# Performance work log

Measured on AMD Instinct MI355X. Metric: run time of the kernel, lower is better.

## Reference

```python
import jax, jax.numpy as jnp
import numpy as np

N_NODES = 50000
N_EDGES = 1600000
HIDDEN = 1024
NUM_CLASSES = 64


def setup_inputs() -> dict:
    key = jax.random.key(0)
    k1, k2, k3 = jax.random.split(key, 3)
    x = jax.random.normal(k1, (N_NODES, HIDDEN), dtype=jnp.float32)
    edge_index = jax.random.randint(k2, (2, N_EDGES), 0, N_NODES, dtype=jnp.int64)
    # Glorot-style init for the GCNConv linear weight, zero bias (PyG defaults)
    W = jax.random.normal(k3, (HIDDEN, NUM_CLASSES), dtype=jnp.float32) / np.sqrt(HIDDEN)
    b = jnp.zeros((NUM_CLASSES,), dtype=jnp.float32)
    return {"x": x, "edge_index": edge_index, "W": W, "b": b}


def reference(x, edge_index, W, b):
    # GCNConv: add self-loops, symmetric deg^{-1/2} normalization,
    # linear transform, gather-scale-scatter aggregation, bias, then softmax.
    n = x.shape[0]
    loops = jnp.arange(n, dtype=edge_index.dtype)
    src = jnp.concatenate([edge_index[0], loops])  # [E+N]
    dst = jnp.concatenate([edge_index[1], loops])  # [E+N]

    ones = jnp.ones(dst.shape[0], dtype=x.dtype)
    deg = jax.ops.segment_sum(ones, dst, num_segments=n)  # in-degree incl. self-loop
    deg_inv_sqrt = jnp.where(deg > 0, jax.lax.rsqrt(deg), 0.0)
    norm = deg_inv_sqrt[src] * deg_inv_sqrt[dst]  # [E+N]

    h = x @ W  # [N, C] dense GEMM (transform before propagate)
    msgs = h[src] * norm[:, None]  # gather + scale
    out = jax.ops.segment_sum(msgs, dst, num_segments=n) + b  # scatter-add
    return jax.nn.softmax(out, axis=1)
```

## Files before the change

### kernel.cpp

```cpp
#include <hip/hip_runtime.h>
#include <hip/hip_bf16.h>
#include <math.h>

#define HIDDEN 1024
#define NCLS 64
#define NB 196
#define BCAP 10240
#define CHUNK 4096
#define GCAP 4096

typedef __attribute__((ext_vector_type(8))) short short8;
typedef __attribute__((ext_vector_type(4))) float f32x4;

__device__ __forceinline__ short f2bf(float f) {
    __hip_bfloat16 b = __float2bfloat16(f);
    return __builtin_bit_cast(short, b);
}
__device__ __forceinline__ float bf2f(short s) {
    unsigned u = ((unsigned)(unsigned short)s) << 16;
    return __builtin_bit_cast(float, u);
}

__device__ __forceinline__ void async_copy16(void* lds, const void* g) {
    __builtin_amdgcn_global_load_lds(
        (const __attribute__((address_space(1))) unsigned int*)g,
        (__attribute__((address_space(3))) unsigned int*)lds, 16, 0, 0);
}

__global__ __launch_bounds__(256) void bucket_kernel(const int* __restrict__ ei,
                                                     unsigned* __restrict__ pairs,
                                                     int* __restrict__ bcnt, int E) {
    __shared__ int hist[256];
    __shared__ int offs[256];
    __shared__ int cur[256];
    __shared__ int gbase[256];
    __shared__ unsigned stage[CHUNK];
    __shared__ int nz;
    __shared__ int wsum[4];
    const int tid = threadIdx.x;
    const int base = blockIdx.x * CHUNK;
    const int cnt_c = min(CHUNK, E - base);

    if (tid == 0) nz = 0;
    hist[tid] = 0;
    cur[tid] = 0;
    __syncthreads();

    int found = 0;
    for (int j = tid; j < 1024; j += 256) {
        int e = base + j;
        if (e < E) found |= (ei[2 * e + 1] != 0);
    }
    if (found) atomicOr(&nz, 1);
    __syncthreads();
    const int is64 = (nz == 0);

    unsigned pr[16];
    #pragma unroll
    for (int j = 0; j < 16; ++j) {
        int e = base + j * 256 + tid;
        unsigned p = 0xFFFFFFFFu;
        if (e < E) {
            int s = is64 ? ei[2 * e] : ei[e];
            int d = is64 ? ei[2 * (E + e)] : ei[E + e];
            p = (unsigned)s | ((unsigned)d << 16);
            atomicAdd(&hist[d >> 8], 1);
        }
        pr[j] = p;
    }
    __syncthreads();

    int v = hist[tid];
    int incl = v;
    #pragma unroll
    for (int d = 1; d < 64; d <<= 1) {
        int t = __shfl_up(incl, d);
        if ((tid & 63) >= d) incl += t;
    }
    if ((tid & 63) == 63) wsum[tid >> 6] = incl;
    __syncthreads();
    int pre = 0;
    #pragma unroll
    for (int w = 0; w < 4; ++w)
        if (w < (tid >> 6)) pre += wsum[w];
    offs[tid] = pre + incl - v;
    if (tid < NB && v > 0) gbase[tid] = atomicAdd(&bcnt[tid], v);
    __syncthreads();

    #pragma unroll
    for (int j = 0; j < 16; ++j) {
        unsigned p = pr[j];
        if (p != 0xFFFFFFFFu) {
            int b = (int)(p >> 24);
            int pos = offs[b] + atomicAdd(&cur[b], 1);
            stage[pos] = p;
        }
    }
    __syncthreads();
    for (int i = tid; i < cnt_c; i += 256) {
        unsigned p = stage[i];
        int b = (int)(p >> 24);
        pairs[(size_t)b * BCAP + gbase[b] + (i - offs[b])] = p;
    }
}

__global__ __launch_bounds__(256) void degree_kernel(const unsigned* __restrict__ pairs,
                                                     const int* __restrict__ bcnt,
                                                     float* __restrict__ dis, int n) {
    __shared__ int hist[256];
    const int tid = threadIdx.x;
    const int bucket = blockIdx.x;
    hist[tid] = 0;
    __syncthreads();
    const int cb = bcnt[bucket];
    const unsigned* bp = pairs + (size_t)bucket * BCAP;
    for (int i = tid; i < cb; i += 256) {
        unsigned p = bp[i];
        atomicAdd(&hist[(p >> 16) & 255], 1);
    }
    __syncthreads();
    int node = bucket * 256 + tid;
    if (node < n) dis[node] = rsqrtf((float)hist[tid] + 1.0f);
}

__global__ void wprep_kernel(const float* __restrict__ W,
                             short* __restrict__ wt_hi, short* __restrict__ wt_lo) {
    int idx = blockIdx.x * 256 + threadIdx.x;
    int c = idx >> 10;
    int k = idx & 1023;
    float f = W[(size_t)k * NCLS + c];
    short hb = f2bf(f);
    wt_hi[idx] = hb;
    wt_lo[idx] = f2bf(f - bf2f(hb));
}

__global__ __launch_bounds__(256) void gemm_mfma_kernel(const float* __restrict__ x,
                                                        const short* __restrict__ wt_hi,
                                                        const short* __restrict__ wt_lo,
                                                        float* __restrict__ h, int M) {
    __shared__ char smem[16 * 1040 + 8 * 1040 + 8 * 1040];
    char* As = smem;
    char* Bh = smem + 16 * 1040;
    char* Bl = smem + 24 * 1040;

    const int tid = threadIdx.x;
    const int wave = tid >> 6;
    const int lane = tid & 63;
    const int l15 = lane & 15, l4 = lane >> 4;
    const int row0 = blockIdx.x * 64;

    const float* agp[4];
    #pragma unroll
    for (int i = 0; i < 4; ++i) {
        int rg = row0 + (wave * 4 + i) * 4 + (lane >> 4);
        if (rg > M - 1) rg = M - 1;
        int g = (lane & 15) ^ (((lane >> 4) & 3) << 2);
        agp[i] = x + (size_t)rg * HIDDEN + g * 4;
    }
    const short* bhp[2];
    const short* blp[2];
    #pragma unroll
    for (int i = 0; i < 2; ++i) {
        int c = (wave * 2 + i) * 8 + (lane >> 3);
        int g = (lane & 7) ^ ((lane >> 3) & 7);
        bhp[i] = wt_hi + (size_t)c * HIDDEN + g * 8;
        blp[i] = wt_lo + (size_t)c * HIDDEN + g * 8;
    }

    f32x4 acc[4];
    #pragma unroll
    for (int nf = 0; nf < 4; ++nf) acc[nf] = (f32x4){0.f, 0.f, 0.f, 0.f};

    const int rt = wave * 16 + l15;
    const int r3 = rt & 3;
    char* arow = As + (rt >> 2) * 1040 + r3 * 256;

    for (int k0 = 0; k0 < HIDDEN; k0 += 64) {
        #pragma unroll
        for (int i = 0; i < 4; ++i)
            async_copy16(As + (wave * 4 + i) * 1040, agp[i] + k0);
        #pragma unroll
        for (int i = 0; i < 2; ++i) {
            async_copy16(Bh + (wave * 2 + i) * 1040, bhp[i] + k0);
            async_copy16(Bl + (wave * 2 + i) * 1040, blp[i] + k0);
        }
        __syncthreads();

        #pragma unroll
        for (int kk = 0; kk < 2; ++kk) {
            int js = (kk * 8 + l4 * 2) ^ (r3 << 2);
            f32x4 af0 = *reinterpret_cast<const f32x4*>(arow + js * 16);
            f32x4 af1 = *reinterpret_cast<const f32x4*>(arow + js * 16 + 16);
            short8 ah, al;
            #pragma unroll
            for (int j = 0; j < 4; ++j) {
                short hb = f2bf(af0[j]);
                ah[j] = hb;
                al[j] = f2bf(af0[j] - bf2f(hb));
                short hb2 = f2bf(af1[j]);
                ah[j + 4] = hb2;
                al[j + 4] = f2bf(af1[j] - bf2f(hb2));
            }
            #pragma unroll
            for (int nf = 0; nf < 4; ++nf) {
                int c = l15 + 16 * nf;
                int jb = (kk * 4 + l4) ^ (c & 7);
                size_t boff = (size_t)(c >> 3) * 1040 + (c & 7) * 128 + jb * 16;
                short8 bh = *reinterpret_cast<const short8*>(Bh + boff);
                short8 bl = *reinterpret_cast<const short8*>(Bl + boff);
                acc[nf] = __builtin_amdgcn_mfma_f32_16x16x32_bf16(ah, bh, acc[nf], 0, 0, 0);
                acc[nf] = __builtin_amdgcn_mfma_f32_16x16x32_bf16(al, bh, acc[nf], 0, 0, 0);
                acc[nf] = __builtin_amdgcn_mfma_f32_16x16x32_bf16(ah, bl, acc[nf], 0, 0, 0);
            }
        }
        __syncthreads();
    }

    #pragma unroll
    for (int j = 0; j < 4; ++j) {
        int r = row0 + wave * 16 + l4 * 4 + j;
        if (r < M) {
            #pragma unroll
            for (int nf = 0; nf < 4; ++nf) {
                h[(size_t)r * NCLS + l15 + 16 * nf] = acc[nf][j];
            }
        }
    }
}

__global__ __launch_bounds__(256) void agg_kernel(const unsigned* __restrict__ pairs,
                                                  const int* __restrict__ bcnt,
                                                  const float* __restrict__ h,
                                                  const float* __restrict__ dis,
                                                  const float* __restrict__ bias,
                                                  float* __restrict__ out, int n) {
    __shared__ int hist[64];
    __shared__ int offs[64];
    __shared__ int cur[64];
    __shared__ unsigned short ssrc[GCAP];
    __shared__ float swt[GCAP];
    const int tid = threadIdx.x;
    const int bucket = blockIdx.x >> 2;
    const int split = blockIdx.x & 3;
    const int base_node = bucket * 256 + split * 64;
    if (base_node >= n) return;
    if (tid < 64) { hist[tid] = 0; cur[tid] = 0; }
    __syncthreads();
    const int cb = bcnt[bucket];
    const unsigned* bp = pairs + (size_t)bucket * BCAP;
    for (int i = tid; i < cb; i += 256) {
        unsigned p = bp[i];
        int loc = (int)((p >> 16) & 255u);
        if ((loc >> 6) == split) atomicAdd(&hist[loc & 63], 1);
    }
    __syncthreads();
    if (tid == 0) {
        int r = 0;
        #pragma unroll
        for (int k = 0; k < 64; ++k) { offs[k] = r; r += hist[k]; }
    }
    __syncthreads();
    for (int i = tid; i < cb; i += 256) {
        unsigned p = bp[i];
        int loc = (int)((p >> 16) & 255u);
        if ((loc >> 6) == split) {
            int ln = loc & 63;
            int pos = offs[ln] + atomicAdd(&cur[ln], 1);
            if (pos < GCAP) {
                int s = (int)(p & 0xFFFFu);
                ssrc[pos] = (unsigned short)s;
                swt[pos] = dis[s];
            }
        }
    }
    __syncthreads();

    const int wave = tid >> 6;
    const int lane = tid & 63;
    const int q = lane & 15;
    const int g = lane >> 4;
    const f32x4 bv = *reinterpret_cast<const f32x4*>(bias + q * 4);

    for (int t = 0; t < 16; ++t) {
        int ln = wave * 16 + t;
        int node = base_node + ln;
        if (node >= n) continue;
        int len = hist[ln];
        int e0 = offs[ln];
        float di = rsqrtf((float)len + 1.0f);

        f32x4 hs = *reinterpret_cast<const f32x4*>(h + (size_t)node * NCLS + q * 4);
        float selfw = (g == 0) ? di : 0.f;
        f32x4 a = {hs[0] * selfw, hs[1] * selfw, hs[2] * selfw, hs[3] * selfw};
        f32x4 a2 = {0.f, 0.f, 0.f, 0.f};

        for (int i = 0; i < len; i += 8) {
            int i1 = i + g;
            bool v1 = i1 < len;
            int s1 = v1 ? (int)ssrc[e0 + i1] : 0;
            float w1 = v1 ? swt[e0 + i1] : 0.f;
            f32x4 r1 = *reinterpret_cast<const f32x4*>(h + (size_t)s1 * NCLS + q * 4);
            if (i + 4 < len) {
                int i2 = i + 4 + g;
                bool v2 = i2 < len;
                int s2 = v2 ? (int)ssrc[e0 + i2] : 0;
                float w2 = v2 ? swt[e0 + i2] : 0.f;
                f32x4 r2 = *reinterpret_cast<const f32x4*>(h + (size_t)s2 * NCLS + q * 4);
                a2[0] += w2 * r2[0]; a2[1] += w2 * r2[1];
                a2[2] += w2 * r2[2]; a2[3] += w2 * r2[3];
            }
            a[0] += w1 * r1[0]; a[1] += w1 * r1[1];
            a[2] += w1 * r1[2]; a[3] += w1 * r1[3];
        }
        #pragma unroll
        for (int c = 0; c < 4; ++c) {
            float s = a[c] + a2[c];
            s += __shfl_xor(s, 16);
            s += __shfl_xor(s, 32);
            a[c] = s * di + bv[c];
        }
        float m = fmaxf(fmaxf(a[0], a[1]), fmaxf(a[2], a[3]));
        #pragma unroll
        for (int d = 1; d < 16; d <<= 1) m = fmaxf(m, __shfl_xor(m, d));
        f32x4 ex;
        #pragma unroll
        for (int c = 0; c < 4; ++c) ex[c] = __expf(a[c] - m);
        float sum = (ex[0] + ex[1]) + (ex[2] + ex[3]);
        #pragma unroll
        for (int d = 1; d < 16; d <<= 1) sum += __shfl_xor(sum, d);
        float inv = 1.f / sum;
        if (g == 0) {
            f32x4 o = {ex[0] * inv, ex[1] * inv, ex[2] * inv, ex[3] * inv};
            *reinterpret_cast<f32x4*>(out + (size_t)node * NCLS + q * 4) = o;
        }
    }
}

extern "C" void kernel_launch(void* const* d_in, const int* in_sizes, int n_in,
                              void* d_out, int out_size, void* d_ws, size_t ws_size,
                              hipStream_t stream) {
    const float* x    = (const float*)d_in[0];
    const int*   ei   = (const int*)d_in[1];
    const float* W    = (const float*)d_in[2];
    const float* bias = (const float*)d_in[3];
    float* out = (float*)d_out;

    const int n = in_sizes[0] / HIDDEN;
    const int E = in_sizes[1] / 2;

    char* ws = (char*)d_ws;
    size_t off = 0;
    auto alloc = [&](size_t bytes) -> void* {
        void* p = (void*)(ws + off);
        off = (off + bytes + 255) & ~((size_t)255);
        return p;
    };
    int*      bcnt  = (int*)alloc((size_t)NB * 4);
    unsigned* pairs = (unsigned*)alloc((size_t)NB * BCAP * 4);
    float*    dis   = (float*)alloc((size_t)n * 4);
    float*    h     = (float*)alloc((size_t)n * NCLS * 4);
    short*    wt_hi = (short*)alloc((size_t)NCLS * HIDDEN * 2);
    short*    wt_lo = (short*)alloc((size_t)NCLS * HIDDEN * 2);
    (void)ws_size;

    hipMemsetAsync(bcnt, 0, (size_t)NB * 4, stream);

    bucket_kernel<<<(E + CHUNK - 1) / CHUNK, 256, 0, stream>>>(ei, pairs, bcnt, E);
    degree_kernel<<<NB, 256, 0, stream>>>(pairs, bcnt, dis, n);

    wprep_kernel<<<(NCLS * HIDDEN) / 256, 256, 0, stream>>>(W, wt_hi, wt_lo);
    gemm_mfma_kernel<<<(n + 63) / 64, 256, 0, stream>>>(x, wt_hi, wt_lo, h, n);
    agg_kernel<<<NB * 4, 256, 0, stream>>>(pairs, bcnt, h, dis, bias, out, n);
}
```

Measured before the change: 164.1 us.

## Co-schedule GEMM and edge bucketing in one launch, store h as fp16

Merges the GEMM and edge-bucketing kernels into one launch that branches on block index, so the memory-bound x read and the edge sort can overlap on the GPU. The intermediate h is now stored in fp16, which halves its write traffic and the gather traffic in aggregation. The aggregation loop switches to 8 lanes per row with 8 channels each. The fp16 h adds rounding error to the result, and the shared-memory buffer is now sized for the larger of the two bodies.

```diff
diff --git a/kernel.cpp b/kernel.cpp
--- a/kernel.cpp
+++ b/kernel.cpp
@@ -1,5 +1,6 @@
 #include <hip/hip_runtime.h>
 #include <hip/hip_bf16.h>
+#include <hip/hip_fp16.h>
 #include <math.h>
 
 #define HIDDEN 1024
@@ -8,9 +9,11 @@
 #define BCAP 10240
 #define CHUNK 4096
 #define GCAP 4096
+#define SMEM_BYTES 33280
 
 typedef __attribute__((ext_vector_type(8))) short short8;
 typedef __attribute__((ext_vector_type(4))) float f32x4;
+typedef __attribute__((ext_vector_type(8))) _Float16 half8;
 
 __device__ __forceinline__ short f2bf(float f) {
     __hip_bfloat16 b = __float2bfloat16(f);
@@ -25,102 +28,6 @@
     __builtin_amdgcn_global_load_lds(
         (const __attribute__((address_space(1))) unsigned int*)g,
         (__attribute__((address_space(3))) unsigned int*)lds, 16, 0, 0);
-}
-
-__global__ __launch_bounds__(256) void bucket_kernel(const int* __restrict__ ei,
-                                                     unsigned* __restrict__ pairs,
-                                                     int* __restrict__ bcnt, int E) {
-    __shared__ int hist[256];
-    __shared__ int offs[256];
-    __shared__ int cur[256];
-    __shared__ int gbase[256];
-    __shared__ unsigned stage[CHUNK];
-    __shared__ int nz;
-    __shared__ int wsum[4];
-    const int tid = threadIdx.x;
-    const int base = blockIdx.x * CHUNK;
-    const int cnt_c = min(CHUNK, E - base);
-
-    if (tid == 0) nz = 0;
-    hist[tid] = 0;
-    cur[tid] = 0;
-    __syncthreads();
-
-    int found = 0;
-    for (int j = tid; j < 1024; j += 256) {
-        int e = base + j;
-        if (e < E) found |= (ei[2 * e + 1] != 0);
-    }
-    if (found) atomicOr(&nz, 1);
-    __syncthreads();
-    const int is64 = (nz == 0);
-
-    unsigned pr[16];
-    #pragma unroll
-    for (int j = 0; j < 16; ++j) {
-        int e = base + j * 256 + tid;
-        unsigned p = 0xFFFFFFFFu;
-        if (e < E) {
-            int s = is64 ? ei[2 * e] : ei[e];
-            int d = is64 ? ei[2 * (E + e)] : ei[E + e];
-            p = (unsigned)s | ((unsigned)d << 16);
-            atomicAdd(&hist[d >> 8], 1);
-        }
-        pr[j] = p;
-    }
-    __syncthreads();
-
-    int v = hist[tid];
-    int incl = v;
-    #pragma unroll
-    for (int d = 1; d < 64; d <<= 1) {
-        int t = __shfl_up(incl, d);
-        if ((tid & 63) >= d) incl += t;
-    }
-    if ((tid & 63) == 63) wsum[tid >> 6] = incl;
-    __syncthreads();
-    int pre = 0;
-    #pragma unroll
-    for (int w = 0; w < 4; ++w)
-        if (w < (tid >> 6)) pre += wsum[w];
-    offs[tid] = pre + incl - v;
-    if (tid < NB && v > 0) gbase[tid] = atomicAdd(&bcnt[tid], v);
-    __syncthreads();
-
-    #pragma unroll
-    for (int j = 0; j < 16; ++j) {
-        unsigned p = pr[j];
-        if (p != 0xFFFFFFFFu) {
-            int b = (int)(p >> 24);
-            int pos = offs[b] + atomicAdd(&cur[b], 1);
-            stage[pos] = p;
-        }
-    }
-    __syncthreads();
-    for (int i = tid; i < cnt_c; i += 256) {
-        unsigned p = stage[i];
-        int b = (int)(p >> 24);
-        pairs[(size_t)b * BCAP + gbase[b] + (i - offs[b])] = p;
-    }
-}
-
-__global__ __launch_bounds__(256) void degree_kernel(const unsigned* __restrict__ pairs,
-                                                     const int* __restrict__ bcnt,
-                                                     float* __restrict__ dis, int n) {
-    __shared__ int hist[256];
-    const int tid = threadIdx.x;
-    const int bucket = blockIdx.x;
-    hist[tid] = 0;
-    __syncthreads();
-    const int cb = bcnt[bucket];
-    const unsigned* bp = pairs + (size_t)bucket * BCAP;
-    for (int i = tid; i < cb; i += 256) {
-        unsigned p = bp[i];
-        atomicAdd(&hist[(p >> 16) & 255], 1);
-    }
-    __syncthreads();
-    int node = bucket * 256 + tid;
-    if (node < n) dis[node] = rsqrtf((float)hist[tid] + 1.0f);
 }
 
 __global__ void wprep_kernel(const float* __restrict__ W,
@@ -134,11 +41,87 @@
     wt_lo[idx] = f2bf(f - bf2f(hb));
 }
 
-__global__ __launch_bounds__(256) void gemm_mfma_kernel(const float* __restrict__ x,
-                                                        const short* __restrict__ wt_hi,
-                                                        const short* __restrict__ wt_lo,
-                                                        float* __restrict__ h, int M) {
-    __shared__ char smem[16 * 1040 + 8 * 1040 + 8 * 1040];
+__device__ void bucket_body(char* smem, const int* __restrict__ ei,
+                            unsigned* __restrict__ pairs, int* __restrict__ bcnt,
+                            int E, int bid) {
+    int* hist = (int*)smem;
+    int* offs = hist + 256;
+    int* cur  = offs + 256;
+    int* gbase = cur + 256;
+    unsigned* stage = (unsigned*)(gbase + 256);
+    int* nz = (int*)(stage + CHUNK);
+    int* wsum = nz + 1;
+
+    const int tid = threadIdx.x;
+    const int base = bid * CHUNK;
+    const int cnt_c = min(CHUNK, E - base);
+
+    if (tid == 0) *nz = 0;
+    hist[tid] = 0;
+    cur[tid] = 0;
+    __syncthreads();
+
+    int found = 0;
+    for (int j = tid; j < 1024; j += 256) {
+        int e = base + j;
+        if (e < E) found |= (ei[2 * e + 1] != 0);
+    }
+    if (found) atomicOr(nz, 1);
+    __syncthreads();
+    const int is64 = (*nz == 0);
+
+    unsigned pr[16];
+    #pragma unroll
+    for (int j = 0; j < 16; ++j) {
+        int e = base + j * 256 + tid;
+        unsigned p = 0xFFFFFFFFu;
+        if (e < E) {
+            int s = is64 ? ei[2 * e] : ei[e];
+            int d = is64 ? ei[2 * (E + e)] : ei[E + e];
+            p = (unsigned)s | ((unsigned)d << 16);
+            atomicAdd(&hist[d >> 8], 1);
+        }
+        pr[j] = p;
+    }
+    __syncthreads();
+
+    int v = hist[tid];
+    int incl = v;
+    #pragma unroll
+    for (int d = 1; d < 64; d <<= 1) {
+        int t = __shfl_up(incl, d);
+        if ((tid & 63) >= d) incl += t;
+    }
+    if ((tid & 63) == 63) wsum[tid >> 6] = incl;
+    __syncthreads();
+    int pre = 0;
+    #pragma unroll
+    for (int w = 0; w < 4; ++w)
+        if (w < (tid >> 6)) pre += wsum[w];
+    offs[tid] = pre + incl - v;
+    if (tid < NB && v > 0) gbase[tid] = atomicAdd(&bcnt[tid], v);
+    __syncthreads();
+
+    #pragma unroll
+    for (int j = 0; j < 16; ++j) {
+        unsigned p = pr[j];
+        if (p != 0xFFFFFFFFu) {
+            int b = (int)(p >> 24);
+            int pos = offs[b] + atomicAdd(&cur[b], 1);
+            stage[pos] = p;
+        }
+    }
+    __syncthreads();
+    for (int i = tid; i < cnt_c; i += 256) {
+        unsigned p = stage[i];
+        int b = (int)(p >> 24);
+        pairs[(size_t)b * BCAP + gbase[b] + (i - offs[b])] = p;
+    }
+}
+
+__device__ void gemm_body(char* smem, const float* __restrict__ x,
+                          const short* __restrict__ wt_hi, const short* __restrict__ wt_lo,
+                          _Float16* __restrict__ h16, int M, int bid) {
     char* As = smem;
     char* Bh = smem + 16 * 1040;
     char* Bl = smem + 24 * 1040;
@@ -147,7 +130,7 @@
     const int wave = tid >> 6;
     const int lane = tid & 63;
     const int l15 = lane & 15, l4 = lane >> 4;
-    const int row0 = blockIdx.x * 64;
+    const int row0 = bid * 64;
 
     const float* agp[4];
     #pragma unroll
@@ -222,15 +205,49 @@
         if (r < M) {
             #pragma unroll
             for (int nf = 0; nf < 4; ++nf) {
-                h[(size_t)r * NCLS + l15 + 16 * nf] = acc[nf][j];
+                h16[(size_t)r * NCLS + l15 + 16 * nf] = (_Float16)acc[nf][j];
             }
         }
     }
+}
+
+__global__ __launch_bounds__(256) void fat_kernel(const float* __restrict__ x,
+                                                  const short* __restrict__ wt_hi,
+                                                  const short* __restrict__ wt_lo,
+                                                  _Float16* __restrict__ h16, int M,
+                                                  const int* __restrict__ ei,
+                                                  unsigned* __restrict__ pairs,
+                                                  int* __restrict__ bcnt, int E,
+                                                  int nGemmBlocks) {
+    __shared__ __align__(16) char smem[SMEM_BYTES];
+    if ((int)blockIdx.x < nGemmBlocks)
+        gemm_body(smem, x, wt_hi, wt_lo, h16, M, blockIdx.x);
+    else
+        bucket_body(smem, ei, pairs, bcnt, E, blockIdx.x - nGemmBlocks);
+}
+
+__global__ __launch_bounds__(256) void degree_kernel(const unsigned* __restrict__ pairs,
+                                                     const int* __restrict__ bcnt,
+                                                     float* __restrict__ dis, int n) {
+    __shared__ int hist[256];
+    const int tid = threadIdx.x;
+    const int bucket = blockIdx.x;
+    hist[tid] = 0;
+    __syncthreads();
+    const int cb = bcnt[bucket];
+    const unsigned* bp = pairs + (size_t)bucket * BCAP;
+    for (int i = tid; i < cb; i += 256) {
+        unsigned p = bp[i];
+        atomicAdd(&hist[(p >> 16) & 255], 1);
+    }
+    __syncthreads();
+    int node = bucket * 256 + tid;
+    if (node < n) dis[node] = rsqrtf((float)hist[tid] + 1.0f);
 }
 
 __global__ __launch_bounds__(256) void agg_kernel(const unsigned* __restrict__ pairs,
                                                   const int* __restrict__ bcnt,
-                                                  const float* __restrict__ h,
+                                                  const _Float16* __restrict__ h16,
                                                   const float* __restrict__ dis,
                                                   const float* __restrict__ bias,
                                                   float* __restrict__ out, int n) {
@@ -277,9 +294,11 @@
 
     const int wave = tid >> 6;
     const int lane = tid & 63;
-    const int q = lane & 15;
-    const int g = lane >> 4;
-    const f32x4 bv = *reinterpret_cast<const f32x4*>(bias + q * 4);
+    const int q = lane & 7;
+    const int g = lane >> 3;
+    float bv[8];
+    #pragma unroll
+    for (int c = 0; c < 8; ++c) bv[c] = bias[q * 8 + c];
 
     for (int t = 0; t < 16; ++t) {
         int ln = wave * 16 + t;
@@ -289,49 +308,54 @@
         int e0 = offs[ln];
         float di = rsqrtf((float)len + 1.0f);
 
-        f32x4 hs = *reinterpret_cast<const f32x4*>(h + (size_t)node * NCLS + q * 4);
+        half8 hs = *reinterpret_cast<const half8*>(h16 + (size_t)node * NCLS + q * 8);
         float selfw = (g == 0) ? di : 0.f;
-        f32x4 a = {hs[0] * selfw, hs[1] * selfw, hs[2] * selfw, hs[3] * selfw};
-        f32x4 a2 = {0.f, 0.f, 0.f, 0.f};
-
-        for (int i = 0; i < len; i += 8) {
+        float a[8], a2[8];
+        #pragma unroll
+        for (int c = 0; c < 8; ++c) { a[c] = (float)hs[c] * selfw; a2[c] = 0.f; }
+
+        for (int i = 0; i < len; i += 16) {
             int i1 = i + g;
             bool v1 = i1 < len;
             int s1 = v1 ? (int)ssrc[e0 + i1] : 0;
             float w1 = v1 ? swt[e0 + i1] : 0.f;
-            f32x4 r1 = *reinterpret_cast<const f32x4*>(h + (size_t)s1 * NCLS + q * 4);
-            if (i + 4 < len) {
-                int i2 = i + 4 + g;
+            half8 r1 = *reinterpret_cast<const half8*>(h16 + (size_t)s1 * NCLS + q * 8);
+            if (i + 8 < len) {
+                int i2 = i + 8 + g;
                 bool v2 = i2 < len;
                 int s2 = v2 ? (int)ssrc[e0 + i2] : 0;
                 float w2 = v2 ? swt[e0 + i2] : 0.f;
-                f32x4 r2 = *reinterpret_cast<const f32x4*>(h + (size_t)s2 * NCLS + q * 4);
-                a2[0] += w2 * r2[0]; a2[1] += w2 * r2[1];
-                a2[2] += w2 * r2[2]; a2[3] += w2 * r2[3];
+                half8 r2 = *reinterpret_cast<const half8*>(h16 + (size_t)s2 * NCLS + q * 8);
+                #pragma unroll
+                for (int c = 0; c < 8; ++c) a2[c] += w2 * (float)r2[c];
             }
-            a[0] += w1 * r1[0]; a[1] += w1 * r1[1];
-            a[2] += w1 * r1[2]; a[3] += w1 * r1[3];
-        }
-        #pragma unroll
-        for (int c = 0; c < 4; ++c) {
+            #pragma unroll
+            for (int c = 0; c < 8; ++c) a[c] += w1 * (float)r1[c];
+        }
+        #pragma unroll
+        for (int c = 0; c < 8; ++c) {
             float s = a[c] + a2[c];
+            s += __shfl_xor(s, 8);
             s += __shfl_xor(s, 16);
             s += __shfl_xor(s, 32);
             a[c] = s * di + bv[c];
         }
-        float m = fmaxf(fmaxf(a[0], a[1]), fmaxf(a[2], a[3]));
-        #pragma unroll
-        for (int d = 1; d < 16; d <<= 1) m = fmaxf(m, __shfl_xor(m, d));
-        f32x4 ex;
-        #pragma unroll
-        for (int c = 0; c < 4; ++c) ex[c] = __expf(a[c] - m);
-        float sum = (ex[0] + ex[1]) + (ex[2] + ex[3]);
-        #pragma unroll
-        for (int d = 1; d < 16; d <<= 1) sum += __shfl_xor(sum, d);
+        float m = a[0];
+        #pragma unroll
+        for (int c = 1; c < 8; ++c) m = fmaxf(m, a[c]);
+        #pragma unroll
+        for (int d = 1; d < 8; d <<= 1) m = fmaxf(m, __shfl_xor(m, d));
+        float ex[8], sum = 0.f;
+        #pragma unroll
+        for (int c = 0; c < 8; ++c) { ex[c] = __expf(a[c] - m); sum += ex[c]; }
+        #pragma unroll
+        for (int d = 1; d < 8; d <<= 1) sum += __shfl_xor(sum, d);
         float inv = 1.f / sum;
         if (g == 0) {
-            f32x4 o = {ex[0] * inv, ex[1] * inv, ex[2] * inv, ex[3] * inv};
-            *reinterpret_cast<f32x4*>(out + (size_t)node * NCLS + q * 4) = o;
+            f32x4 o0 = {ex[0] * inv, ex[1] * inv, ex[2] * inv, ex[3] * inv};
+            f32x4 o1 = {ex[4] * inv, ex[5] * inv, ex[6] * inv, ex[7] * inv};
+            *reinterpret_cast<f32x4*>(out + (size_t)node * NCLS + q * 8) = o0;
+            *reinterpret_cast<f32x4*>(out + (size_t)node * NCLS + q * 8 + 4) = o1;
         }
     }
 }
@@ -358,17 +382,20 @@
     int*      bcnt  = (int*)alloc((size_t)NB * 4);
     unsigned* pairs = (unsigned*)alloc((size_t)NB * BCAP * 4);
     float*    dis   = (float*)alloc((size_t)n * 4);
-    float*    h     = (float*)alloc((size_t)n * NCLS * 4);
+    _Float16* h16   = (_Float16*)alloc((size_t)n * NCLS * 2);
     short*    wt_hi = (short*)alloc((size_t)NCLS * HIDDEN * 2);
     short*    wt_lo = (short*)alloc((size_t)NCLS * HIDDEN * 2);
     (void)ws_size;
 
     hipMemsetAsync(bcnt, 0, (size_t)NB * 4, stream);
 
-    bucket_kernel<<<(E + CHUNK - 1) / CHUNK, 256, 0, stream>>>(ei, pairs, bcnt, E);
+    wprep_kernel<<<(NCLS * HIDDEN) / 256, 256, 0, stream>>>(W, wt_hi, wt_lo);
+
+    const int nGemmBlocks = (n + 63) / 64;
+    const int nBucketBlocks = (E + CHUNK - 1) / CHUNK;
+    fat_kernel<<<nGemmBlocks + nBucketBlocks, 256, 0, stream>>>(
+        x, wt_hi, wt_lo, h16, n, ei, pairs, bcnt, E, nGemmBlocks);
+
     degree_kernel<<<NB, 256, 0, stream>>>(pairs, bcnt, dis, n);
-
-    wprep_kernel<<<(NCLS * HIDDEN) / 256, 256, 0, stream>>>(W, wt_hi, wt_lo);
-    gemm_mfma_kernel<<<(n + 63) / 64, 256, 0, stream>>>(x, wt_hi, wt_lo, h, n);
-    agg_kernel<<<NB * 4, 256, 0, stream>>>(pairs, bcnt, h, dis, bias, out, n);
-}
+    agg_kernel<<<NB * 4, 256, 0, stream>>>(pairs, bcnt, h16, dis, bias, out, n);
+}
```

Result: faster. 135.3 us (-17.6%).
